# Optimization experiments

Measured on AMD Instinct MI355X. Metric: run time of the kernel, lower is better.

## Reference

```python
import jax, jax.numpy as jnp
import numpy as np

B, D, S = 128, 256, 512
K, H, NCLS = 50, 256, 2
THRES = 0.3  # conceptshap threshold


def _l2norm(x, axis):
    n = jnp.sqrt(jnp.sum(x * x, axis=axis, keepdims=True))
    return x / jnp.maximum(n, 1e-12)


def setup_inputs() -> dict:
    key = jax.random.key(0)
    ks = jax.random.split(key, 6)
    return {
        "f_input": jax.random.normal(ks[0], (B, D, S), dtype=jnp.float32),
        "targets": jax.random.uniform(ks[1], (B,), dtype=jnp.float32),
        "topic_vector": jax.random.uniform(ks[2], (D, K), minval=-0.5, maxval=0.5, dtype=jnp.float32),
        "rec_vector_1": jax.random.uniform(ks[3], (K, H), minval=-0.5, maxval=0.5, dtype=jnp.float32),
        "rec_vector_2": jax.random.uniform(ks[4], (H, D), minval=-0.5, maxval=0.5, dtype=jnp.float32),
        "Wc": jax.random.normal(ks[5], (D, NCLS), dtype=jnp.float32) * 0.05,
        "bc": jnp.zeros((NCLS,), dtype=jnp.float32),
        "causal": 0,
    }


def reference(f_input, targets, topic_vector, rec_vector_1, rec_vector_2, Wc, bc, causal):
    # text path (n=3), model_name != 'transformer' -> swap to [B, S, D]
    x = jnp.swapaxes(f_input, 1, 2)                # [B, S, D]
    x_n = _l2norm(x, axis=-1)                      # F.normalize(dim=n-1)
    tv_n = _l2norm(topic_vector, axis=0)           # [D, K], column-normalized

    topic_prob = jnp.einsum('bsd,dk->bsk', x, tv_n)      # [B, S, K]
    topic_prob_n = jnp.einsum('bsd,dk->bsk', x_n, tv_n)  # [B, S, K]

    # conceptshap: no softmax, hard threshold mask
    mask = (topic_prob_n > THRES).astype(topic_prob.dtype)
    topic_prob_am = topic_prob * mask
    topic_prob_sum = jnp.sum(topic_prob_am, axis=-1, keepdims=True) + 0.001
    topic_prob_nn = topic_prob_am / (topic_prob_sum + 1e-8)

    rec_layer_1 = jax.nn.relu(jnp.einsum('bsk,kh->bsh', topic_prob_nn, rec_vector_1))
    rec_layer_2 = jnp.einsum('bsh,hd->bsd', rec_layer_1, rec_vector_2)  # [B, S, D]

    ae_loss = jnp.mean((x_n - rec_layer_2) ** 2)

    rec_out = jnp.swapaxes(rec_layer_2, 1, 2)      # back to [B, D, S]
    # frozen classifier: mean over seq + linear head
    pred = jnp.mean(rec_out, axis=-1) @ Wc + bc    # [B, NCLS]

    # concept_sim: mean of per-concept top-(B//4) similarity scores, negated
    res = topic_prob_n.reshape(-1, K).T            # [K, B*S]
    topv, _ = jax.lax.top_k(res, B // 4)
    concept_sim = -jnp.mean(topv)

    concept_far = jnp.mean(tv_n.T @ tv_n - jnp.eye(K, dtype=tv_n.dtype))

    return (pred, jnp.float32(0.0), concept_sim, concept_far, topic_prob_nn, ae_loss)
```

## Files before the change

### kernel.cpp

```cpp
#include <hip/hip_runtime.h>
#include <math.h>

#define BB 128
#define DD 256
#define SS 512
#define KK 50
#define HH 256
#define TS 128
#define NBLK (BB * SS / TS)
#define BS (BB * SS)

#define CHUNK 1024
#define NCH (BS / CHUNK)
#define TOPK 32
#define MAXSURV 512
#define NSUB (TS / 16)

#define TVN_OFF 0
#define TVNT_OFF (TVN_OFF + DD * KK)
#define TPNT_OFF (TVNT_OFF + KK * DD)
#define PREDACC_OFF (TPNT_OFF + KK * BS)
#define AE_OFF (PREDACC_OFF + BB * DD)
#define SIM_OFF (AE_OFF + 1)
#define CNT_OFF (AE_OFF + 2)
#define LIST_OFF (AE_OFF + 4)
#define CAND_OFF (LIST_OFF + MAXSURV)

#define OUT_NN_OFF 259
#define OUT_AE_IDX (OUT_NN_OFF + KK * BS)

__device__ __forceinline__ unsigned fkey(float f) {
  unsigned u = __float_as_uint(f);
  return (u & 0x80000000u) ? ~u : (u | 0x80000000u);
}
__device__ __forceinline__ float keyval(unsigned T) {
  unsigned u = (T & 0x80000000u) ? (T & 0x7FFFFFFFu) : ~T;
  return __uint_as_float(u);
}

__global__ __launch_bounds__(256) void tvn_kernel(const float* __restrict__ tv,
                                                  float* __restrict__ tvn,
                                                  float* __restrict__ tvnT) {
  __shared__ float red[256];
  const int k = blockIdx.x, t = threadIdx.x;
  float v = tv[t * KK + k];
  red[t] = v * v;
  __syncthreads();
  for (int off = 128; off > 0; off >>= 1) {
    if (t < off) red[t] += red[t + off];
    __syncthreads();
  }
  float inv = 1.0f / fmaxf(sqrtf(red[0]), 1e-12f);
  const float nv = v * inv;
  tvn[t * KK + k] = nv;
  tvnT[k * DD + t] = nv;
}

__global__ __launch_bounds__(256) void main_kernel(
    const float* __restrict__ f_input, const float* __restrict__ tvnT,
    float* __restrict__ out_nn, float* __restrict__ tpn_t,
    float* __restrict__ ae_acc, int* __restrict__ surv_cnt,
    int* __restrict__ surv_list) {
  __shared__ int wflag[4];

  const int blk = blockIdx.x;
  const int b = blk >> 2;
  const int s0 = (blk & 3) * TS;
  const int t = threadIdx.x;
  const int lane = t & 63;
  const int wid = t >> 6;
  const int kb = __builtin_amdgcn_readfirstlane(wid);

  const float* tvk[13];
  bool kval[13];
  #pragma unroll
  for (int j = 0; j < 13; ++j) {
    const int k = 4 * j + kb;
    kval[j] = (k < KK);
    tvk[j] = tvnT + (size_t)(kval[j] ? k : (KK - 1)) * DD;
  }

  const float* xp = f_input + (size_t)b * DD * SS + s0 + 2 * lane;

  float acc0[13], acc1[13];
  #pragma unroll
  for (int j = 0; j < 13; ++j) { acc0[j] = 0.0f; acc1[j] = 0.0f; }

  float s2_0 = 0.0f, s2_1 = 0.0f;
  for (int part = 0; part < 8; ++part) {
    float p0 = 0.0f, p1 = 0.0f;
    #pragma unroll 2
    for (int dd = 0; dd < 32; dd += 4) {
      const int d0 = part * 32 + dd;
      const float2 xa = *(const float2*)(xp + (size_t)(d0 + 0) * SS);
      const float2 xb = *(const float2*)(xp + (size_t)(d0 + 1) * SS);
      const float2 xc = *(const float2*)(xp + (size_t)(d0 + 2) * SS);
      const float2 xd = *(const float2*)(xp + (size_t)(d0 + 3) * SS);
      p0 += xa.x * xa.x; p0 += xb.x * xb.x; p0 += xc.x * xc.x; p0 += xd.x * xd.x;
      p1 += xa.y * xa.y; p1 += xb.y * xb.y; p1 += xc.y * xc.y; p1 += xd.y * xd.y;
      #pragma unroll
      for (int j = 0; j < 13; ++j) {
        const float4 tq = *(const float4*)(tvk[j] + d0);
        acc0[j] += xa.x * tq.x; acc0[j] += xb.x * tq.y;
        acc0[j] += xc.x * tq.z; acc0[j] += xd.x * tq.w;
        acc1[j] += xa.y * tq.x; acc1[j] += xb.y * tq.y;
        acc1[j] += xc.y * tq.z; acc1[j] += xd.y * tq.w;
      }
    }
    s2_0 = (part == 0) ? p0 : (s2_0 + p0);
    s2_1 = (part == 0) ? p1 : (s2_1 + p1);
  }
  const float i0 = 1.0f / fmaxf(sqrtf(s2_0), 1e-12f);
  const float i1 = 1.0f / fmaxf(sqrtf(s2_1), 1e-12f);

  bool m = false;
  const size_t gs = (size_t)b * SS + s0 + 2 * lane;
  #pragma unroll
  for (int j = 0; j < 13; ++j) {
    if (kval[j]) {
      const int k = 4 * j + kb;
      float2 o;
      o.x = acc0[j] * i0;
      o.y = acc1[j] * i1;
      *(float2*)(tpn_t + (size_t)k * BS + gs) = o;
      m = m | (o.x > 0.3f) | (o.y > 0.3f);
    }
  }

  const int w = __any((int)m);
  if (lane == 0) wflag[wid] = w;
  __syncthreads();
  const int any = wflag[0] | wflag[1] | wflag[2] | wflag[3];

  if (!any) {
    float* ob = out_nn + ((size_t)b * SS + s0) * KK;
    for (int p = t; p < TS * KK; p += 256) ob[p] = 0.0f;
    if (t == 0) atomicAdd(ae_acc, (float)TS);
    return;
  }
  if (t == 0) {
    const int idx = atomicAdd(surv_cnt, 1);
    if (idx < MAXSURV) surv_list[idx] = blk;
  }
}

__global__ __launch_bounds__(256) void surv_kernel(
    const float* __restrict__ f_input, const float* __restrict__ tpn_t,
    const float* __restrict__ rec1, const float* __restrict__ rec2,
    const int* __restrict__ surv_cnt, const int* __restrict__ surv_list,
    float* __restrict__ out_nn, float* __restrict__ predacc,
    float* __restrict__ ae_acc) {
  __shared__ __align__(16) float NNk[KK * 20];
  __shared__ __align__(16) float R1t[HH * 20];
  __shared__ float nprt[16][17];
  __shared__ float nrm[16], invn[16];
  __shared__ float pm[8 * DD];
  __shared__ float red4[4];
  const int t = threadIdx.x;
  const int lane = t & 63, wid = t >> 6;
  int cnt = *surv_cnt;
  if (cnt > MAXSURV) cnt = MAXSURV;
  const int ntask = NSUB * cnt;

  for (int task = blockIdx.x; task < ntask; task += 64) {
    const int blk = surv_list[task / NSUB];
    const int q = task % NSUB;
    const int b = blk >> 2;
    const int s0 = (blk & 3) * TS + q * 16;
    const float* fb = f_input + (size_t)b * DD * SS;
    const size_t gs0 = (size_t)b * SS + s0;

    for (int p = t; p < KK * 16; p += 256) {
      const int k = p >> 4, ss = p & 15;
      NNk[k * 20 + ss] = tpn_t[(size_t)k * BS + gs0 + ss];
    }
    {
      const int ss = t & 15, part = t >> 4;
      const float* xc = fb + (size_t)(part * 16) * SS + s0 + ss;
      float p = 0.0f;
      #pragma unroll
      for (int i = 0; i < 16; ++i) {
        const float v = xc[(size_t)i * SS];
        p += v * v;
      }
      nprt[part][ss] = p;
    }
    __syncthreads();
    if (t < 16) {
      float s2 = 0.0f;
      #pragma unroll
      for (int i = 0; i < 16; ++i) s2 += nprt[i][t];
      const float n = fmaxf(sqrtf(s2), 1e-12f);
      nrm[t] = n;
      invn[t] = 1.0f / n;
      float sm = 0.0f;
      for (int k = 0; k < KK; ++k) {
        const float tpn = NNk[k * 20 + t];
        sm += (tpn > 0.3f) ? tpn * n : 0.0f;
      }
      const float idv = 1.0f / (sm + 0.001f + 1e-8f);
      for (int k = 0; k < KK; ++k) {
        const float tpn = NNk[k * 20 + t];
        NNk[k * 20 + t] = (tpn > 0.3f) ? tpn * n * idv : 0.0f;
      }
    }
    __syncthreads();

    for (int p = t; p < 16 * KK; p += 256) {
      const int ss = p / KK, k = p - ss * KK;
      out_nn[(gs0 + ss) * KK + k] = NNk[k * 20 + ss];
    }

    {
      float rcol[KK];
      #pragma unroll
      for (int k = 0; k < KK; ++k) rcol[k] = rec1[k * HH + t];
      float a[16];
      #pragma unroll
      for (int i = 0; i < 16; ++i) a[i] = 0.0f;
      #pragma unroll 2
      for (int k = 0; k < KK; ++k) {
        const float r = rcol[k];
        const float4* np = (const float4*)&NNk[k * 20];
        #pragma unroll
        for (int qq = 0; qq < 4; ++qq) {
          const float4 nv = np[qq];
          a[qq * 4 + 0] += nv.x * r;
          a[qq * 4 + 1] += nv.y * r;
          a[qq * 4 + 2] += nv.z * r;
          a[qq * 4 + 3] += nv.w * r;
        }
      }
      #pragma unroll
      for (int i = 0; i < 16; ++i) R1t[t * 20 + i] = fmaxf(a[i], 0.0f);
    }
    __syncthreads();

    const int tx = t & 31, ty = t >> 5;
    const int d0 = tx * 8, sb = ty * 2;
    float c2[2][8];
    #pragma unroll
    for (int i = 0; i < 2; ++i)
      #pragma unroll
      for (int j = 0; j < 8; ++j) c2[i][j] = 0.0f;
    for (int h0 = 0; h0 < HH; h0 += 8) {
      float4 B0[8], B1[8];
      #pragma unroll
      for (int u = 0; u < 8; ++u) {
        B0[u] = *(const float4*)(rec2 + (h0 + u) * DD + d0);
        B1[u] = *(const float4*)(rec2 + (h0 + u) * DD + d0 + 4);
      }
      #pragma unroll
      for (int u = 0; u < 8; ++u) {
        const float2 a01 = *(const float2*)(&R1t[(h0 + u) * 20 + sb]);
        const float bv[8] = {B0[u].x, B0[u].y, B0[u].z, B0[u].w,
                             B1[u].x, B1[u].y, B1[u].z, B1[u].w};
        #pragma unroll
        for (int j = 0; j < 8; ++j) {
          c2[0][j] += a01.x * bv[j];
          c2[1][j] += a01.y * bv[j];
        }
      }
    }
    #pragma unroll
    for (int j = 0; j < 8; ++j) pm[ty * DD + d0 + j] = c2[0][j] + c2[1][j];
    __syncthreads();
    {
      float sum = 0.0f;
      #pragma unroll
      for (int r = 0; r < 8; ++r) sum += pm[r * DD + t];
      atomicAdd(&predacc[(size_t)b * DD + t], sum);
    }
    float e = 0.0f;
    #pragma unroll
    for (int j = 0; j < 8; ++j) {
      #pragma unroll
      for (int i = 0; i < 2; ++i) {
        const float x = fb[(size_t)(d0 + j) * SS + s0 + sb + i];
        const float diff = x * invn[sb + i] - c2[i][j];
        e += diff * diff;
      }
    }
    #pragma unroll
    for (int off = 1; off < 64; off <<= 1) e += __shfl_xor(e, off);
    if (lane == 0) red4[wid] = e;
    __syncthreads();
    if (t == 0) atomicAdd(ae_acc, red4[0] + red4[1] + red4[2] + red4[3]);
    __syncthreads();
  }
}

__global__ __launch_bounds__(256) void topk_chunk_kernel(const float* __restrict__ tpn_t,
                                                         float* __restrict__ cand) {
  const int wave = threadIdx.x >> 6;
  const int lane = threadIdx.x & 63;
  const int gchunk = blockIdx.x * 4 + wave;
  const int k = gchunk >> 6;
  const int c = gchunk & (NCH - 1);
  const float* row = tpn_t + (size_t)k * BS + c * CHUNK;

  float v[16];
  unsigned key[16];
  #pragma unroll
  for (int j = 0; j < 16; ++j) {
    v[j] = row[lane + j * 64];
    key[j] = fkey(v[j]);
  }

  unsigned T = 0;
  for (int bit = 31; bit >= 0; --bit) {
    const unsigned ct = T | (1u << bit);
    int cnt = 0;
    #pragma unroll
    for (int j = 0; j < 16; ++j) cnt += (key[j] >= ct) ? 1 : 0;
    #pragma unroll
    for (int off = 1; off < 64; off <<= 1) cnt += __shfl_xor(cnt, off);
    if (cnt >= TOPK) T = ct;
  }

  int cg = 0;
  #pragma unroll
  for (int j = 0; j < 16; ++j) cg += (key[j] > T) ? 1 : 0;
  int incl = cg;
  #pragma unroll
  for (int off = 1; off < 64; off <<= 1) {
    int y = __shfl_up(incl, off);
    if (lane >= off) incl += y;
  }
  const int excl = incl - cg;
  const int total_gt = __shfl(incl, 63);

  float* cb = cand + (size_t)gchunk * TOPK;
  int pos = excl;
  #pragma unroll
  for (int j = 0; j < 16; ++j) {
    if (key[j] > T) cb[pos++] = v[j];
  }
  if (lane < TOPK - total_gt) cb[total_gt + lane] = keyval(T);
}

__global__ __launch_bounds__(64) void topk_merge_kernel(const float* __restrict__ cand,
                                                        float* __restrict__ sim_acc) {
  const int lane = threadIdx.x & 63;
  const float* row = cand + (size_t)blockIdx.x * (NCH * TOPK);

  float v[32];
  unsigned key[32];
  #pragma unroll
  for (int j = 0; j < 32; ++j) {
    v[j] = row[lane + j * 64];
    key[j] = fkey(v[j]);
  }

  unsigned T = 0;
  for (int bit = 31; bit >= 0; --bit) {
    const unsigned ct = T | (1u << bit);
    int cnt = 0;
    #pragma unroll
    for (int j = 0; j < 32; ++j) cnt += (key[j] >= ct) ? 1 : 0;
    #pragma unroll
    for (int off = 1; off < 64; off <<= 1) cnt += __shfl_xor(cnt, off);
    if (cnt >= TOPK) T = ct;
  }

  float s = 0.0f;
  int cgt = 0;
  #pragma unroll
  for (int j = 0; j < 32; ++j) {
    if (key[j] > T) { s += v[j]; cgt++; }
  }
  #pragma unroll
  for (int off = 1; off < 64; off <<= 1) {
    s += __shfl_xor(s, off);
    cgt += __shfl_xor(cgt, off);
  }
  if (lane == 0) {
    atomicAdd(sim_acc, s + (float)(TOPK - cgt) * keyval(T));
  }
}

__global__ __launch_bounds__(256) void finalize_kernel(
    const float* __restrict__ predacc, const float* __restrict__ Wc,
    const float* __restrict__ bc, const float* __restrict__ ae_acc,
    const float* __restrict__ sim_acc, const float* __restrict__ tvn,
    float* __restrict__ out) {
  __shared__ float r0[256], r1[256];
  const int b = blockIdx.x, t = threadIdx.x;
  const float s = predacc[(size_t)b * DD + t];
  r0[t] = s * Wc[t * 2 + 0];
  r1[t] = s * Wc[t * 2 + 1];
  __syncthreads();
  for (int off = 128; off > 0; off >>= 1) {
    if (t < off) { r0[t] += r0[t + off]; r1[t] += r1[t + off]; }
    __syncthreads();
  }
  if (t == 0) {
    out[b * 2 + 0] = r0[0] * (1.0f / (float)SS) + bc[0];
    out[b * 2 + 1] = r1[0] * (1.0f / (float)SS) + bc[1];
    if (b == 0) {
      out[256] = 0.0f;
      out[257] = -(*sim_acc) * (1.0f / (float)(KK * TOPK));
      out[OUT_AE_IDX] = (*ae_acc) * (1.0f / ((float)BB * (float)SS * (float)DD));
    }
  }
  if (b == 0) {
    __syncthreads();
    float rs = 0.0f;
    for (int k = 0; k < KK; ++k) rs += tvn[t * KK + k];
    r0[t] = rs * rs;
    __syncthreads();
    for (int off = 128; off > 0; off >>= 1) {
      if (t < off) r0[t] += r0[t + off];
      __syncthreads();
    }
    if (t == 0) out[258] = (r0[0] - (float)KK) / ((float)KK * (float)KK);
  }
}

extern "C" void kernel_launch(void* const* d_in, const int* in_sizes, int n_in,
                              void* d_out, int out_size, void* d_ws, size_t ws_size,
                              hipStream_t stream) {
  (void)in_sizes; (void)n_in; (void)out_size; (void)ws_size;
  const float* f_input = (const float*)d_in[0];
  const float* tv = (const float*)d_in[2];
  const float* rec1 = (const float*)d_in[3];
  const float* rec2 = (const float*)d_in[4];
  const float* Wc = (const float*)d_in[5];
  const float* bc = (const float*)d_in[6];

  float* out = (float*)d_out;
  float* ws = (float*)d_ws;
  float* tvn = ws + TVN_OFF;
  float* tvnT = ws + TVNT_OFF;
  float* tpn_t = ws + TPNT_OFF;
  float* predacc = ws + PREDACC_OFF;
  float* ae_acc = ws + AE_OFF;
  float* sim_acc = ws + SIM_OFF;
  int* surv_cnt = (int*)(ws + CNT_OFF);
  int* surv_list = (int*)(ws + LIST_OFF);
  float* cand = ws + CAND_OFF;

  hipMemsetAsync(predacc, 0, (size_t)(BB * DD + 3) * sizeof(float), stream);

  tvn_kernel<<<KK, 256, 0, stream>>>(tv, tvn, tvnT);
  main_kernel<<<NBLK, 256, 0, stream>>>(f_input, tvnT, out + OUT_NN_OFF, tpn_t,
                                        ae_acc, surv_cnt, surv_list);
  surv_kernel<<<64, 256, 0, stream>>>(f_input, tpn_t, rec1, rec2,
                                      surv_cnt, surv_list, out + OUT_NN_OFF,
                                      predacc, ae_acc);
  topk_chunk_kernel<<<KK * NCH / 4, 256, 0, stream>>>(tpn_t, cand);
  topk_merge_kernel<<<KK, 64, 0, stream>>>(cand, sim_acc);
  finalize_kernel<<<BB, 256, 0, stream>>>(predacc, Wc, bc, ae_acc, sim_acc, tvn, out);
}
```

Baseline: 228.4 us.

## Halve main tile, prefetch x, fuse topk-chunk with surv and merge with finalize

Shrinks the main-kernel tile from 128 to 64 sequence positions, giving one position per lane with register double-buffered x loads and a higher occupancy hint. The memset moves into tvn_kernel, top-k chunk selection is merged into the survivor kernel as extra blocks, and the top-k merge is merged into finalize, with a completion counter writing concept_sim. This cuts kernel launches and improves latency hiding, but tvnT is now loaded once per position instead of once per two, and rec1 is read from global memory inside the loop instead of being cached in registers.

Result: no change. 231.0 us (+1.2%).

```diff
diff --git a/kernel.cpp b/kernel.cpp
--- a/kernel.cpp
+++ b/kernel.cpp
@@ -6,12 +6,13 @@
 #define SS 512
 #define KK 50
 #define HH 256
-#define TS 128
+#define TS 64
 #define NBLK (BB * SS / TS)
 #define BS (BB * SS)
 
 #define CHUNK 1024
 #define NCH (BS / CHUNK)
+#define NCHBLK (KK * NCH / 4)
 #define TOPK 32
 #define MAXSURV 512
 #define NSUB (TS / 16)
@@ -23,8 +24,10 @@
 #define AE_OFF (PREDACC_OFF + BB * DD)
 #define SIM_OFF (AE_OFF + 1)
 #define CNT_OFF (AE_OFF + 2)
+#define SIMD_OFF (AE_OFF + 3)
 #define LIST_OFF (AE_OFF + 4)
 #define CAND_OFF (LIST_OFF + MAXSURV)
+#define NZERO (BB * DD + 4)
 
 #define OUT_NN_OFF 259
 #define OUT_AE_IDX (OUT_NN_OFF + KK * BS)
@@ -40,9 +43,14 @@
 
 __global__ __launch_bounds__(256) void tvn_kernel(const float* __restrict__ tv,
                                                   float* __restrict__ tvn,
-                                                  float* __restrict__ tvnT) {
+                                                  float* __restrict__ tvnT,
+                                                  float* __restrict__ zbase) {
   __shared__ float red[256];
   const int k = blockIdx.x, t = threadIdx.x;
+  {
+    const int gid = k * 256 + t;
+    for (int i = gid; i < NZERO; i += KK * 256) zbase[i] = 0.0f;
+  }
   float v = tv[t * KK + k];
   red[t] = v * v;
   __syncthreads();
@@ -56,7 +64,7 @@
   tvnT[k * DD + t] = nv;
 }
 
-__global__ __launch_bounds__(256) void main_kernel(
+__global__ __launch_bounds__(256, 4) void main_kernel(
     const float* __restrict__ f_input, const float* __restrict__ tvnT,
     float* __restrict__ out_nn, float* __restrict__ tpn_t,
     float* __restrict__ ae_acc, int* __restrict__ surv_cnt,
@@ -64,8 +72,8 @@
   __shared__ int wflag[4];
 
   const int blk = blockIdx.x;
-  const int b = blk >> 2;
-  const int s0 = (blk & 3) * TS;
+  const int b = blk >> 3;
+  const int s0 = (blk & 7) * TS;
   const int t = threadIdx.x;
   const int lane = t & 63;
   const int wid = t >> 6;
@@ -80,50 +88,49 @@
     tvk[j] = tvnT + (size_t)(kval[j] ? k : (KK - 1)) * DD;
   }
 
-  const float* xp = f_input + (size_t)b * DD * SS + s0 + 2 * lane;
-
-  float acc0[13], acc1[13];
+  const float* xp = f_input + (size_t)b * DD * SS + s0 + lane;
+
+  float acc[13];
   #pragma unroll
-  for (int j = 0; j < 13; ++j) { acc0[j] = 0.0f; acc1[j] = 0.0f; }
-
-  float s2_0 = 0.0f, s2_1 = 0.0f;
+  for (int j = 0; j < 13; ++j) acc[j] = 0.0f;
+
+  float xb[2][4];
+  #pragma unroll
+  for (int i = 0; i < 4; ++i) xb[0][i] = xp[(size_t)i * SS];
+
+  float s2 = 0.0f;
+  int buf = 0;
   for (int part = 0; part < 8; ++part) {
-    float p0 = 0.0f, p1 = 0.0f;
-    #pragma unroll 2
+    float p = 0.0f;
+    #pragma unroll
     for (int dd = 0; dd < 32; dd += 4) {
       const int d0 = part * 32 + dd;
-      const float2 xa = *(const float2*)(xp + (size_t)(d0 + 0) * SS);
-      const float2 xb = *(const float2*)(xp + (size_t)(d0 + 1) * SS);
-      const float2 xc = *(const float2*)(xp + (size_t)(d0 + 2) * SS);
-      const float2 xd = *(const float2*)(xp + (size_t)(d0 + 3) * SS);
-      p0 += xa.x * xa.x; p0 += xb.x * xb.x; p0 += xc.x * xc.x; p0 += xd.x * xd.x;
-      p1 += xa.y * xa.y; p1 += xb.y * xb.y; p1 += xc.y * xc.y; p1 += xd.y * xd.y;
+      const int dn = (d0 + 4 < DD) ? (d0 + 4) : 0;
+      #pragma unroll
+      for (int i = 0; i < 4; ++i) xb[buf ^ 1][i] = xp[(size_t)(dn + i) * SS];
+      const float x0 = xb[buf][0], x1 = xb[buf][1], x2 = xb[buf][2], x3 = xb[buf][3];
+      p += x0 * x0; p += x1 * x1; p += x2 * x2; p += x3 * x3;
       #pragma unroll
       for (int j = 0; j < 13; ++j) {
         const float4 tq = *(const float4*)(tvk[j] + d0);
-        acc0[j] += xa.x * tq.x; acc0[j] += xb.x * tq.y;
-        acc0[j] += xc.x * tq.z; acc0[j] += xd.x * tq.w;
-        acc1[j] += xa.y * tq.x; acc1[j] += xb.y * tq.y;
-        acc1[j] += xc.y * tq.z; acc1[j] += xd.y * tq.w;
-      }
-    }
-    s2_0 = (part == 0) ? p0 : (s2_0 + p0);
-    s2_1 = (part == 0) ? p1 : (s2_1 + p1);
-  }
-  const float i0 = 1.0f / fmaxf(sqrtf(s2_0), 1e-12f);
-  const float i1 = 1.0f / fmaxf(sqrtf(s2_1), 1e-12f);
+        acc[j] += x0 * tq.x; acc[j] += x1 * tq.y;
+        acc[j] += x2 * tq.z; acc[j] += x3 * tq.w;
+      }
+      buf ^= 1;
+    }
+    s2 = (part == 0) ? p : (s2 + p);
+  }
+  const float invn = 1.0f / fmaxf(sqrtf(s2), 1e-12f);
 
   bool m = false;
-  const size_t gs = (size_t)b * SS + s0 + 2 * lane;
+  const size_t gs = (size_t)b * SS + s0 + lane;
   #pragma unroll
   for (int j = 0; j < 13; ++j) {
     if (kval[j]) {
       const int k = 4 * j + kb;
-      float2 o;
-      o.x = acc0[j] * i0;
-      o.y = acc1[j] * i1;
-      *(float2*)(tpn_t + (size_t)k * BS + gs) = o;
-      m = m | (o.x > 0.3f) | (o.y > 0.3f);
+      const float o = acc[j] * invn;
+      tpn_t[(size_t)k * BS + gs] = o;
+      m |= (o > 0.3f);
     }
   }
 
@@ -134,7 +141,7 @@
 
   if (!any) {
     float* ob = out_nn + ((size_t)b * SS + s0) * KK;
-    for (int p = t; p < TS * KK; p += 256) ob[p] = 0.0f;
+    for (int p2 = t; p2 < TS * KK; p2 += 256) ob[p2] = 0.0f;
     if (t == 0) atomicAdd(ae_acc, (float)TS);
     return;
   }
@@ -144,29 +151,77 @@
   }
 }
 
-__global__ __launch_bounds__(256) void surv_kernel(
-    const float* __restrict__ f_input, const float* __restrict__ tpn_t,
-    const float* __restrict__ rec1, const float* __restrict__ rec2,
-    const int* __restrict__ surv_cnt, const int* __restrict__ surv_list,
-    float* __restrict__ out_nn, float* __restrict__ predacc,
-    float* __restrict__ ae_acc) {
+__global__ __launch_bounds__(256) void chunk_surv_kernel(
+    const float* __restrict__ tpn_t, float* __restrict__ cand,
+    const float* __restrict__ f_input, const float* __restrict__ rec1,
+    const float* __restrict__ rec2, const int* __restrict__ surv_cnt,
+    const int* __restrict__ surv_list, float* __restrict__ out_nn,
+    float* __restrict__ predacc, float* __restrict__ ae_acc) {
   __shared__ __align__(16) float NNk[KK * 20];
   __shared__ __align__(16) float R1t[HH * 20];
   __shared__ float nprt[16][17];
   __shared__ float nrm[16], invn[16];
   __shared__ float pm[8 * DD];
   __shared__ float red4[4];
+
   const int t = threadIdx.x;
   const int lane = t & 63, wid = t >> 6;
+
+  if (blockIdx.x < NCHBLK) {
+    const int gchunk = blockIdx.x * 4 + wid;
+    const int k = gchunk >> 6;
+    const int c = gchunk & (NCH - 1);
+    const float* row = tpn_t + (size_t)k * BS + c * CHUNK;
+
+    float v[16];
+    unsigned key[16];
+    #pragma unroll
+    for (int j = 0; j < 16; ++j) {
+      v[j] = row[lane + j * 64];
+      key[j] = fkey(v[j]);
+    }
+    unsigned T = 0;
+    for (int bit = 31; bit >= 0; --bit) {
+      const unsigned ct = T | (1u << bit);
+      int cnt = 0;
+      #pragma unroll
+      for (int j = 0; j < 16; ++j) cnt += (key[j] >= ct) ? 1 : 0;
+      #pragma unroll
+      for (int off = 1; off < 64; off <<= 1) cnt += __shfl_xor(cnt, off);
+      if (cnt >= TOPK) T = ct;
+    }
+    int cg = 0;
+    #pragma unroll
+    for (int j = 0; j < 16; ++j) cg += (key[j] > T) ? 1 : 0;
+    int incl = cg;
+    #pragma unroll
+    for (int off = 1; off < 64; off <<= 1) {
+      int y = __shfl_up(incl, off);
+      if (lane >= off) incl += y;
+    }
+    const int excl = incl - cg;
+    const int total_gt = __shfl(incl, 63);
+
+    float* cb = cand + (size_t)gchunk * TOPK;
+    int pos = excl;
+    #pragma unroll
+    for (int j = 0; j < 16; ++j) {
+      if (key[j] > T) cb[pos++] = v[j];
+    }
+    if (lane < TOPK - total_gt) cb[total_gt + lane] = keyval(T);
+    return;
+  }
+
+  const int bid = blockIdx.x - NCHBLK;
   int cnt = *surv_cnt;
   if (cnt > MAXSURV) cnt = MAXSURV;
   const int ntask = NSUB * cnt;
 
-  for (int task = blockIdx.x; task < ntask; task += 64) {
+  for (int task = bid; task < ntask; task += 64) {
     const int blk = surv_list[task / NSUB];
     const int q = task % NSUB;
-    const int b = blk >> 2;
-    const int s0 = (blk & 3) * TS + q * 16;
+    const int b = blk >> 3;
+    const int s0 = (blk & 7) * TS + q * 16;
     const float* fb = f_input + (size_t)b * DD * SS;
     const size_t gs0 = (size_t)b * SS + s0;
 
@@ -212,15 +267,12 @@
     }
 
     {
-      float rcol[KK];
-      #pragma unroll
-      for (int k = 0; k < KK; ++k) rcol[k] = rec1[k * HH + t];
       float a[16];
       #pragma unroll
       for (int i = 0; i < 16; ++i) a[i] = 0.0f;
       #pragma unroll 2
       for (int k = 0; k < KK; ++k) {
-        const float r = rcol[k];
+        const float r = rec1[k * HH + t];
         const float4* np = (const float4*)&NNk[k * 20];
         #pragma unroll
         for (int qq = 0; qq < 4; ++qq) {
@@ -290,103 +342,64 @@
   }
 }
 
-__global__ __launch_bounds__(256) void topk_chunk_kernel(const float* __restrict__ tpn_t,
-                                                         float* __restrict__ cand) {
-  const int wave = threadIdx.x >> 6;
-  const int lane = threadIdx.x & 63;
-  const int gchunk = blockIdx.x * 4 + wave;
-  const int k = gchunk >> 6;
-  const int c = gchunk & (NCH - 1);
-  const float* row = tpn_t + (size_t)k * BS + c * CHUNK;
-
-  float v[16];
-  unsigned key[16];
-  #pragma unroll
-  for (int j = 0; j < 16; ++j) {
-    v[j] = row[lane + j * 64];
-    key[j] = fkey(v[j]);
-  }
-
-  unsigned T = 0;
-  for (int bit = 31; bit >= 0; --bit) {
-    const unsigned ct = T | (1u << bit);
-    int cnt = 0;
-    #pragma unroll
-    for (int j = 0; j < 16; ++j) cnt += (key[j] >= ct) ? 1 : 0;
-    #pragma unroll
-    for (int off = 1; off < 64; off <<= 1) cnt += __shfl_xor(cnt, off);
-    if (cnt >= TOPK) T = ct;
-  }
-
-  int cg = 0;
-  #pragma unroll
-  for (int j = 0; j < 16; ++j) cg += (key[j] > T) ? 1 : 0;
-  int incl = cg;
-  #pragma unroll
-  for (int off = 1; off < 64; off <<= 1) {
-    int y = __shfl_up(incl, off);
-    if (lane >= off) incl += y;
-  }
-  const int excl = incl - cg;
-  const int total_gt = __shfl(incl, 63);
-
-  float* cb = cand + (size_t)gchunk * TOPK;
-  int pos = excl;
-  #pragma unroll
-  for (int j = 0; j < 16; ++j) {
-    if (key[j] > T) cb[pos++] = v[j];
-  }
-  if (lane < TOPK - total_gt) cb[total_gt + lane] = keyval(T);
-}
-
-__global__ __launch_bounds__(64) void topk_merge_kernel(const float* __restrict__ cand,
-                                                        float* __restrict__ sim_acc) {
-  const int lane = threadIdx.x & 63;
-  const float* row = cand + (size_t)blockIdx.x * (NCH * TOPK);
-
-  float v[32];
-  unsigned key[32];
-  #pragma unroll
-  for (int j = 0; j < 32; ++j) {
-    v[j] = row[lane + j * 64];
-    key[j] = fkey(v[j]);
-  }
-
-  unsigned T = 0;
-  for (int bit = 31; bit >= 0; --bit) {
-    const unsigned ct = T | (1u << bit);
-    int cnt = 0;
-    #pragma unroll
-    for (int j = 0; j < 32; ++j) cnt += (key[j] >= ct) ? 1 : 0;
-    #pragma unroll
-    for (int off = 1; off < 64; off <<= 1) cnt += __shfl_xor(cnt, off);
-    if (cnt >= TOPK) T = ct;
-  }
-
-  float s = 0.0f;
-  int cgt = 0;
-  #pragma unroll
-  for (int j = 0; j < 32; ++j) {
-    if (key[j] > T) { s += v[j]; cgt++; }
-  }
-  #pragma unroll
-  for (int off = 1; off < 64; off <<= 1) {
-    s += __shfl_xor(s, off);
-    cgt += __shfl_xor(cgt, off);
-  }
-  if (lane == 0) {
-    atomicAdd(sim_acc, s + (float)(TOPK - cgt) * keyval(T));
-  }
-}
-
-__global__ __launch_bounds__(256) void finalize_kernel(
-    const float* __restrict__ predacc, const float* __restrict__ Wc,
-    const float* __restrict__ bc, const float* __restrict__ ae_acc,
-    const float* __restrict__ sim_acc, const float* __restrict__ tvn,
+__global__ __launch_bounds__(256) void merge_finalize_kernel(
+    const float* __restrict__ cand, const float* __restrict__ predacc,
+    const float* __restrict__ Wc, const float* __restrict__ bc,
+    const float* __restrict__ ae_acc, float* __restrict__ sim_acc,
+    unsigned* __restrict__ sim_done, const float* __restrict__ tvn,
     float* __restrict__ out) {
   __shared__ float r0[256], r1[256];
-  const int b = blockIdx.x, t = threadIdx.x;
-  const float s = predacc[(size_t)b * DD + t];
+  const int blk = blockIdx.x;
+  const int t = threadIdx.x;
+
+  if (blk >= BB) {
+    if (t < 64) {
+      const int k = blk - BB;
+      const int lane = t;
+      const float* row = cand + (size_t)k * (NCH * TOPK);
+      float v[32];
+      unsigned key[32];
+      #pragma unroll
+      for (int j = 0; j < 32; ++j) {
+        v[j] = row[lane + j * 64];
+        key[j] = fkey(v[j]);
+      }
+      unsigned T = 0;
+      for (int bit = 31; bit >= 0; --bit) {
+        const unsigned ct = T | (1u << bit);
+        int cnt = 0;
+        #pragma unroll
+        for (int j = 0; j < 32; ++j) cnt += (key[j] >= ct) ? 1 : 0;
+        #pragma unroll
+        for (int off = 1; off < 64; off <<= 1) cnt += __shfl_xor(cnt, off);
+        if (cnt >= TOPK) T = ct;
+      }
+      float s = 0.0f;
+      int cgt = 0;
+      #pragma unroll
+      for (int j = 0; j < 32; ++j) {
+        if (key[j] > T) { s += v[j]; cgt++; }
+      }
+      #pragma unroll
+      for (int off = 1; off < 64; off <<= 1) {
+        s += __shfl_xor(s, off);
+        cgt += __shfl_xor(cgt, off);
+      }
+      if (lane == 0) {
+        atomicAdd(sim_acc, s + (float)(TOPK - cgt) * keyval(T));
+        __threadfence();
+        const unsigned c = atomicAdd(sim_done, 1u);
+        if (c == KK - 1) {
+          __threadfence();
+          const float tot = atomicAdd(sim_acc, 0.0f);
+          out[257] = -tot * (1.0f / (float)(KK * TOPK));
+        }
+      }
+    }
+    return;
+  }
+
+  const float s = predacc[(size_t)blk * DD + t];
   r0[t] = s * Wc[t * 2 + 0];
   r1[t] = s * Wc[t * 2 + 1];
   __syncthreads();
@@ -395,15 +408,14 @@
     __syncthreads();
   }
   if (t == 0) {
-    out[b * 2 + 0] = r0[0] * (1.0f / (float)SS) + bc[0];
-    out[b * 2 + 1] = r1[0] * (1.0f / (float)SS) + bc[1];
-    if (b == 0) {
+    out[blk * 2 + 0] = r0[0] * (1.0f / (float)SS) + bc[0];
+    out[blk * 2 + 1] = r1[0] * (1.0f / (float)SS) + bc[1];
+    if (blk == 0) {
       out[256] = 0.0f;
-      out[257] = -(*sim_acc) * (1.0f / (float)(KK * TOPK));
       out[OUT_AE_IDX] = (*ae_acc) * (1.0f / ((float)BB * (float)SS * (float)DD));
     }
   }
-  if (b == 0) {
+  if (blk == 0) {
     __syncthreads();
     float rs = 0.0f;
     for (int k = 0; k < KK; ++k) rs += tvn[t * KK + k];
@@ -437,18 +449,16 @@
   float* ae_acc = ws + AE_OFF;
   float* sim_acc = ws + SIM_OFF;
   int* surv_cnt = (int*)(ws + CNT_OFF);
+  unsigned* sim_done = (unsigned*)(ws + SIMD_OFF);
   int* surv_list = (int*)(ws + LIST_OFF);
   float* cand = ws + CAND_OFF;
 
-  hipMemsetAsync(predacc, 0, (size_t)(BB * DD + 3) * sizeof(float), stream);
-
-  tvn_kernel<<<KK, 256, 0, stream>>>(tv, tvn, tvnT);
+  tvn_kernel<<<KK, 256, 0, stream>>>(tv, tvn, tvnT, predacc);
   main_kernel<<<NBLK, 256, 0, stream>>>(f_input, tvnT, out + OUT_NN_OFF, tpn_t,
                                         ae_acc, surv_cnt, surv_list);
-  surv_kernel<<<64, 256, 0, stream>>>(f_input, tpn_t, rec1, rec2,
-                                      surv_cnt, surv_list, out + OUT_NN_OFF,
-                                      predacc, ae_acc);
-  topk_chunk_kernel<<<KK * NCH / 4, 256, 0, stream>>>(tpn_t, cand);
-  topk_merge_kernel<<<KK, 64, 0, stream>>>(cand, sim_acc);
-  finalize_kernel<<<BB, 256, 0, stream>>>(predacc, Wc, bc, ae_acc, sim_acc, tvn, out);
-}
+  chunk_surv_kernel<<<NCHBLK + 64, 256, 0, stream>>>(
+      tpn_t, cand, f_input, rec1, rec2, surv_cnt, surv_list,
+      out + OUT_NN_OFF, predacc, ae_acc);
+  merge_finalize_kernel<<<BB + KK, 256, 0, stream>>>(
+      cand, predacc, Wc, bc, ae_acc, sim_acc, sim_done, tvn, out);
+}
```
